# Kernel tuning notes

Measured on AMD Instinct MI355X. Metric: run time of the kernel, lower is better.

## Reference

```python
import jax, jax.numpy as jnp
import numpy as np

B, C_IN, C_OUT, A, H, W = 32, 256, 512, 256, 64, 64


def setup_inputs() -> dict:
    key = jax.random.key(0)
    ks = jax.random.split(key, 8)
    s = 0.02
    return {
        "x": jax.random.normal(ks[0], (B, C_IN, H, W), dtype=jnp.float32),
        "g": jax.random.normal(ks[1], (B, C_OUT), dtype=jnp.float32),
        "Wg": jax.random.normal(ks[2], (A, C_OUT), dtype=jnp.float32) * s,
        "bg": jnp.full((A,), 0.1, dtype=jnp.float32),
        "Wx": jax.random.normal(ks[3], (A, C_IN), dtype=jnp.float32) * s,
        "bx": jnp.full((A,), 0.1, dtype=jnp.float32),
        "Wf": jax.random.normal(ks[4], (1, A), dtype=jnp.float32) * s,
        "bf": jnp.full((1,), 0.1, dtype=jnp.float32),
    }


def reference(x, g, Wg, bg, Wx, bx, Wf, bf):
    b, c, h, w = x.shape
    gg = g @ Wg.T + bg                                  # [B, A]
    xf = x.reshape(b, c, h * w)                          # [B, C, HW]
    # Linear_x applied per spatial position (batched instead of python loop)
    nx = jnp.einsum('bcn,ac->bna', xf, Wx) + bx          # [B, HW, A]
    nx = jax.nn.relu(gg[:, None, :] + nx)                # [B, HW, A]
    att = jnp.einsum('bna,a->bn', nx, Wf[0]) + bf[0]     # [B, HW]
    # min-subtract, sum-divide normalization
    att = att - jnp.min(att, axis=1, keepdims=True)
    att = att / jnp.sum(att, axis=1, keepdims=True)
    out = jnp.einsum('bcn,bn->bc', xf, att)              # weighted pooling [B, C]
    return out, att.reshape(b, h, w)
```

## Files before the change

### kernel.cpp

```cpp
#include <hip/hip_runtime.h>
#include <stdint.h>

#define B_   32
#define CIN  256
#define COUT 512
#define A_   256
#define HW_  4096
#define NT   64

typedef short  short8  __attribute__((ext_vector_type(8)));
typedef float  float4_ __attribute__((ext_vector_type(4)));

__device__ __forceinline__ unsigned f2bf(float f) {
    unsigned u = __float_as_uint(f);
    u += 0x7FFFu + ((u >> 16) & 1u);
    return u >> 16;
}
__device__ __forceinline__ float bf2f(unsigned h) {
    return __uint_as_float(h << 16);
}

__global__ __launch_bounds__(256) void prep_kernel(
    const float* __restrict__ g, const float* __restrict__ Wg,
    const float* __restrict__ bg, const float* __restrict__ Wx,
    const float* __restrict__ bx,
    uint4* __restrict__ WxR, float* __restrict__ ggbx,
    float* __restrict__ P, float* __restrict__ T)
{
    int t = threadIdx.x;
    if (blockIdx.x >= 32) {
        int e = (blockIdx.x - 32) * 256 + t;
        int lane = e & 63, ai = (e >> 6) & 3, kk = (e >> 8) & 7, w = e >> 11;
        int a  = w * 64 + ai * 16 + (lane & 15);
        int kb = kk * 32 + (lane >> 4) * 8;
        const float4* s = (const float4*)(Wx + (size_t)a * 256 + kb);
        float4 u0 = s[0], u1 = s[1];
        uint4 pk;
        pk.x = f2bf(u0.x) | (f2bf(u0.y) << 16);
        pk.y = f2bf(u0.z) | (f2bf(u0.w) << 16);
        pk.z = f2bf(u1.x) | (f2bf(u1.y) << 16);
        pk.w = f2bf(u1.z) | (f2bf(u1.w) << 16);
        WxR[e] = pk;
        return;
    }
    int b = blockIdx.x;
    int i = b * 256 + t;
    P[i] = 0.f; T[i] = 0.f;

    __shared__ float gl[COUT];
    gl[t]       = g[b * COUT + t];
    gl[t + 256] = g[b * COUT + 256 + t];
    __syncthreads();

    float acc0 = bg[t] + bx[t], acc1 = 0.f;
    const float4* wr = (const float4*)(Wg + (size_t)t * COUT);
    #pragma unroll 8
    for (int co = 0; co < COUT / 4; co += 2) {
        float4 wv0 = wr[co],     gv0 = *(const float4*)&gl[co * 4];
        float4 wv1 = wr[co + 1], gv1 = *(const float4*)&gl[co * 4 + 4];
        acc0 += wv0.x * gv0.x + wv0.y * gv0.y + wv0.z * gv0.z + wv0.w * gv0.w;
        acc1 += wv1.x * gv1.x + wv1.y * gv1.y + wv1.z * gv1.z + wv1.w * gv1.w;
    }
    ggbx[b * 256 + t] = acc0 + acc1;
}

__global__ __launch_bounds__(256, 4) void attn_main(
    const float* __restrict__ x, const char* __restrict__ WxR,
    const float* __restrict__ ggbx, const float* __restrict__ Wf,
    const float* __restrict__ bfs,
    float* __restrict__ P, float* __restrict__ T, float* __restrict__ raw)
{
    __shared__ unsigned int xT[NT * 128];
    __shared__ float att_part[4][NT];
    __shared__ float raw_l[NT];

    int bid = blockIdx.x;
    int b = bid >> 6, nt = bid & 63;
    int t = threadIdx.x, w = t >> 6, lane = t & 63;
    int quad = lane >> 4, l15 = lane & 15;

    const float* xb = x + (size_t)b * CIN * HW_ + nt * NT;

    {
        int sub = lane >> 4;
        int n4  = (lane & 15) * 4;
        int cb0 = w * 64 + sub * 8;
        int cb1 = cb0 + 32;
        float4_ v[16];
        #pragma unroll
        for (int j = 0; j < 8; j++)
            v[j] = *(const float4_*)(xb + (size_t)(cb0 + j) * HW_ + n4);
        #pragma unroll
        for (int j = 0; j < 8; j++)
            v[8 + j] = *(const float4_*)(xb + (size_t)(cb1 + j) * HW_ + n4);

        #pragma unroll
        for (int gq = 0; gq < 2; gq++) {
            int q = (gq ? cb1 : cb0) >> 3;
            const float4_* vg = &v[gq * 8];
            #pragma unroll
            for (int r = 0; r < 4; r++) {
                uint4 pk;
                pk.x = f2bf(vg[0][r]) | (f2bf(vg[1][r]) << 16);
                pk.y = f2bf(vg[2][r]) | (f2bf(vg[3][r]) << 16);
                pk.z = f2bf(vg[4][r]) | (f2bf(vg[5][r]) << 16);
                pk.w = f2bf(vg[6][r]) | (f2bf(vg[7][r]) << 16);
                int n = n4 + r;
                *(uint4*)&xT[n * 128 + ((q ^ (n & 31)) << 2)] = pk;
            }
        }
    }

    float ga[4], wfv[4];
    #pragma unroll
    for (int ai = 0; ai < 4; ai++) {
        int a = w * 64 + ai * 16 + l15;
        ga[ai]  = ggbx[b * 256 + a];
        wfv[ai] = Wf[a];
    }
    __syncthreads();

    float4_ acc[4][4];
    #pragma unroll
    for (int mi = 0; mi < 4; mi++)
        #pragma unroll
        for (int ai = 0; ai < 4; ai++)
            acc[mi][ai] = (float4_){0.f, 0.f, 0.f, 0.f};

    const char* wsl = WxR + w * 32768 + lane * 16;
    short8 afA[4], bfA[4], afB[4], bfB[4];

    auto LD = [&](short8* af, short8* bf, int k0) {
        int qk = (k0 >> 3) + quad;
        #pragma unroll
        for (int mi = 0; mi < 4; mi++) {
            int n = mi * 16 + l15;
            af[mi] = *(const short8*)&xT[n * 128 + ((qk ^ (n & 31)) << 2)];
        }
        const char* wk = wsl + (k0 >> 5) * 4096;
        #pragma unroll
        for (int ai = 0; ai < 4; ai++)
            bf[ai] = *(const short8*)(wk + ai * 1024);
    };
    auto MM = [&](short8* af, short8* bf) {
        #pragma unroll
        for (int mi = 0; mi < 4; mi++)
            #pragma unroll
            for (int ai = 0; ai < 4; ai++)
                acc[mi][ai] = __builtin_amdgcn_mfma_f32_16x16x32_bf16(
                    af[mi], bf[ai], acc[mi][ai], 0, 0, 0);
    };

    LD(afA, bfA, 0);   LD(afB, bfB, 32);
    MM(afA, bfA);      LD(afA, bfA, 64);
    MM(afB, bfB);      LD(afB, bfB, 96);
    MM(afA, bfA);      LD(afA, bfA, 128);
    MM(afB, bfB);      LD(afB, bfB, 160);
    MM(afA, bfA);      LD(afA, bfA, 192);
    MM(afB, bfB);      LD(afB, bfB, 224);
    MM(afA, bfA);
    MM(afB, bfB);

    #pragma unroll
    for (int mi = 0; mi < 4; mi++) {
        float p[4] = {0.f, 0.f, 0.f, 0.f};
        #pragma unroll
        for (int ai = 0; ai < 4; ai++) {
            #pragma unroll
            for (int r = 0; r < 4; r++) {
                float vv = acc[mi][ai][r] + ga[ai];
                vv = fmaxf(vv, 0.f);
                p[r] = fmaf(vv, wfv[ai], p[r]);
            }
        }
        #pragma unroll
        for (int r = 0; r < 4; r++) {
            #pragma unroll
            for (int off = 1; off < 16; off <<= 1)
                p[r] += __shfl_xor(p[r], off, 16);
        }
        if (l15 == 0) {
            #pragma unroll
            for (int r = 0; r < 4; r++)
                att_part[w][mi * 16 + quad * 4 + r] = p[r];
        }
    }
    __syncthreads();

    if (t < NT) {
        float rv = att_part[0][t] + att_part[1][t] + att_part[2][t] + att_part[3][t] + bfs[0];
        raw[b * HW_ + nt * NT + t] = rv;
        raw_l[t] = rv;
    }
    __syncthreads();

    float pp[4] = {0.f, 0.f, 0.f, 0.f};
    float tt[4] = {0.f, 0.f, 0.f, 0.f};
    {
        int q    = (t & 63) >> 1;
        int half = (t & 1) * 8;
        int nb   = (t >> 6) * 16;
        #pragma unroll
        for (int i = 0; i < 16; i++) {
            int n = nb + i;
            uint2 u = *(const uint2*)((const char*)xT + n * 512 + ((q ^ (n & 31)) << 4) + half);
            float rv = raw_l[n];
            float x0 = bf2f(u.x & 0xFFFFu), x1 = bf2f(u.x >> 16);
            float x2 = bf2f(u.y & 0xFFFFu), x3 = bf2f(u.y >> 16);
            pp[0] = fmaf(x0, rv, pp[0]); tt[0] += x0;
            pp[1] = fmaf(x1, rv, pp[1]); tt[1] += x1;
            pp[2] = fmaf(x2, rv, pp[2]); tt[2] += x2;
            pp[3] = fmaf(x3, rv, pp[3]); tt[3] += x3;
        }
    }
    __syncthreads();
    {
        float* red = (float*)xT;
        float4_* pr = (float4_*)(red + w * 512);
        float4_* tr = (float4_*)(red + w * 512 + 256);
        pr[t & 63] = (float4_){pp[0], pp[1], pp[2], pp[3]};
        tr[t & 63] = (float4_){tt[0], tt[1], tt[2], tt[3]};
        __syncthreads();
        float Pc = red[t] + red[512 + t] + red[1024 + t] + red[1536 + t];
        float Tc = red[256 + t] + red[768 + t] + red[1280 + t] + red[1792 + t];
        atomicAdd(&P[b * 256 + t], Pc);
        atomicAdd(&T[b * 256 + t], Tc);
    }
}

__global__ __launch_bounds__(256) void finalize_kernel(
    const float* __restrict__ raw, const float* __restrict__ P,
    const float* __restrict__ T, float* __restrict__ out)
{
    int b = blockIdx.x, t = threadIdx.x;
    const float* r = raw + (size_t)b * HW_;
    float v[16];
    float mn = 3.4e38f, sm = 0.f;
    #pragma unroll
    for (int i = 0; i < 16; i++) {
        v[i] = r[t + 256 * i];
        mn = fminf(mn, v[i]);
        sm += v[i];
    }
    #pragma unroll
    for (int off = 1; off < 64; off <<= 1) {
        mn = fminf(mn, __shfl_xor(mn, off, 64));
        sm += __shfl_xor(sm, off, 64);
    }
    __shared__ float smn[4], ssm[4];
    int w = t >> 6;
    if ((t & 63) == 0) { smn[w] = mn; ssm[w] = sm; }
    __syncthreads();
    mn = fminf(fminf(smn[0], smn[1]), fminf(smn[2], smn[3]));
    sm = (ssm[0] + ssm[1]) + (ssm[2] + ssm[3]);
    float S = sm - 4096.f * mn;
    float inv = 1.f / S;

    float* att = out + B_ * CIN + (size_t)b * HW_;
    #pragma unroll
    for (int i = 0; i < 16; i++) att[t + 256 * i] = (v[i] - mn) * inv;

    int ic = b * 256 + t;
    out[ic] = (P[ic] - mn * T[ic]) * inv;
}

extern "C" void kernel_launch(void* const* d_in, const int* in_sizes, int n_in,
                              void* d_out, int out_size, void* d_ws, size_t ws_size,
                              hipStream_t stream)
{
    const float* x   = (const float*)d_in[0];
    const float* g   = (const float*)d_in[1];
    const float* Wg  = (const float*)d_in[2];
    const float* bg  = (const float*)d_in[3];
    const float* Wx  = (const float*)d_in[4];
    const float* bx  = (const float*)d_in[5];
    const float* Wf  = (const float*)d_in[6];
    const float* bf  = (const float*)d_in[7];
    float* out = (float*)d_out;

    char* wsb = (char*)d_ws;
    uint4* WxR  = (uint4*)wsb;
    float* ggbx = (float*)(wsb + 131072);
    float* P    = ggbx + 8192;
    float* T    = P + 8192;
    float* raw  = T + 8192;

    prep_kernel<<<64, 256, 0, stream>>>(g, Wg, bg, Wx, bx, WxR, ggbx, P, T);
    attn_main<<<2048, 256, 0, stream>>>(x, (const char*)WxR, ggbx, Wf, bf, P, T, raw);
    finalize_kernel<<<32, 256, 0, stream>>>(raw, P, T, out);
}
```

Measured before the change: 243.7 us.

## Make attention kernel persistent over 8 tiles with register-resident Wx and double-buffered x

Each block now handles 8 consecutive spatial tiles of 64 positions with 512 threads (8 waves) instead of one tile with 256 threads. Each wave keeps its slice of the bf16 Wx fragments in registers for the whole block rather than reloading them every tile. The next tile's x values are loaded into registers and written into a second LDS buffer while the current tile is processed, so global loads overlap compute. Per-block atomics to P and T also drop eightfold. In exchange the grid shrinks to 256 blocks, which lowers parallelism and occupancy on a large GPU, and register pressure rises.

```diff
diff --git a/kernel.cpp b/kernel.cpp
--- a/kernel.cpp
+++ b/kernel.cpp
@@ -7,6 +7,7 @@
 #define A_   256
 #define HW_  4096
 #define NT   64
+#define TILES 8
 
 typedef short  short8  __attribute__((ext_vector_type(8)));
 typedef float  float4_ __attribute__((ext_vector_type(4)));
@@ -64,146 +65,153 @@
     ggbx[b * 256 + t] = acc0 + acc1;
 }
 
-__global__ __launch_bounds__(256, 4) void attn_main(
+__global__ __launch_bounds__(512, 2) void attn_main(
     const float* __restrict__ x, const char* __restrict__ WxR,
     const float* __restrict__ ggbx, const float* __restrict__ Wf,
     const float* __restrict__ bfs,
     float* __restrict__ P, float* __restrict__ T, float* __restrict__ raw)
 {
-    __shared__ unsigned int xT[NT * 128];
-    __shared__ float att_part[4][NT];
+    __shared__ unsigned int xT[2][NT * 128];
+    __shared__ float att_part[8][NT];
     __shared__ float raw_l[NT];
 
     int bid = blockIdx.x;
-    int b = bid >> 6, nt = bid & 63;
+    int b = bid >> 3, tg = bid & 7;
     int t = threadIdx.x, w = t >> 6, lane = t & 63;
     int quad = lane >> 4, l15 = lane & 15;
 
-    const float* xb = x + (size_t)b * CIN * HW_ + nt * NT;
-
+    const float* xb = x + (size_t)b * CIN * HW_ + tg * (TILES * NT);
+
+    short8 bfp[16];
     {
-        int sub = lane >> 4;
-        int n4  = (lane & 15) * 4;
-        int cb0 = w * 64 + sub * 8;
-        int cb1 = cb0 + 32;
-        float4_ v[16];
-        #pragma unroll
-        for (int j = 0; j < 8; j++)
-            v[j] = *(const float4_*)(xb + (size_t)(cb0 + j) * HW_ + n4);
-        #pragma unroll
-        for (int j = 0; j < 8; j++)
-            v[8 + j] = *(const float4_*)(xb + (size_t)(cb1 + j) * HW_ + n4);
-
-        #pragma unroll
-        for (int gq = 0; gq < 2; gq++) {
-            int q = (gq ? cb1 : cb0) >> 3;
-            const float4_* vg = &v[gq * 8];
-            #pragma unroll
-            for (int r = 0; r < 4; r++) {
-                uint4 pk;
-                pk.x = f2bf(vg[0][r]) | (f2bf(vg[1][r]) << 16);
-                pk.y = f2bf(vg[2][r]) | (f2bf(vg[3][r]) << 16);
-                pk.z = f2bf(vg[4][r]) | (f2bf(vg[5][r]) << 16);
-                pk.w = f2bf(vg[6][r]) | (f2bf(vg[7][r]) << 16);
-                int n = n4 + r;
-                *(uint4*)&xT[n * 128 + ((q ^ (n & 31)) << 2)] = pk;
-            }
-        }
-    }
-
-    float ga[4], wfv[4];
-    #pragma unroll
-    for (int ai = 0; ai < 4; ai++) {
-        int a = w * 64 + ai * 16 + l15;
+        const char* wsl = WxR + (w >> 1) * 32768 + (w & 1) * 2048 + lane * 16;
+        #pragma unroll
+        for (int kk = 0; kk < 8; kk++) {
+            bfp[kk * 2]     = *(const short8*)(wsl + kk * 4096);
+            bfp[kk * 2 + 1] = *(const short8*)(wsl + kk * 4096 + 1024);
+        }
+    }
+
+    float ga[2], wfv[2];
+    #pragma unroll
+    for (int ai = 0; ai < 2; ai++) {
+        int a = w * 32 + ai * 16 + l15;
         ga[ai]  = ggbx[b * 256 + a];
         wfv[ai] = Wf[a];
     }
-    __syncthreads();
-
-    float4_ acc[4][4];
-    #pragma unroll
-    for (int mi = 0; mi < 4; mi++)
-        #pragma unroll
-        for (int ai = 0; ai < 4; ai++)
-            acc[mi][ai] = (float4_){0.f, 0.f, 0.f, 0.f};
-
-    const char* wsl = WxR + w * 32768 + lane * 16;
-    short8 afA[4], bfA[4], afB[4], bfB[4];
-
-    auto LD = [&](short8* af, short8* bf, int k0) {
-        int qk = (k0 >> 3) + quad;
-        #pragma unroll
-        for (int mi = 0; mi < 4; mi++) {
-            int n = mi * 16 + l15;
-            af[mi] = *(const short8*)&xT[n * 128 + ((qk ^ (n & 31)) << 2)];
-        }
-        const char* wk = wsl + (k0 >> 5) * 4096;
-        #pragma unroll
-        for (int ai = 0; ai < 4; ai++)
-            bf[ai] = *(const short8*)(wk + ai * 1024);
-    };
-    auto MM = [&](short8* af, short8* bf) {
-        #pragma unroll
-        for (int mi = 0; mi < 4; mi++)
-            #pragma unroll
-            for (int ai = 0; ai < 4; ai++)
-                acc[mi][ai] = __builtin_amdgcn_mfma_f32_16x16x32_bf16(
-                    af[mi], bf[ai], acc[mi][ai], 0, 0, 0);
-    };
-
-    LD(afA, bfA, 0);   LD(afB, bfB, 32);
-    MM(afA, bfA);      LD(afA, bfA, 64);
-    MM(afB, bfB);      LD(afB, bfB, 96);
-    MM(afA, bfA);      LD(afA, bfA, 128);
-    MM(afB, bfB);      LD(afB, bfB, 160);
-    MM(afA, bfA);      LD(afA, bfA, 192);
-    MM(afB, bfB);      LD(afB, bfB, 224);
-    MM(afA, bfA);
-    MM(afB, bfB);
-
-    #pragma unroll
-    for (int mi = 0; mi < 4; mi++) {
-        float p[4] = {0.f, 0.f, 0.f, 0.f};
-        #pragma unroll
-        for (int ai = 0; ai < 4; ai++) {
-            #pragma unroll
-            for (int r = 0; r < 4; r++) {
-                float vv = acc[mi][ai][r] + ga[ai];
-                vv = fmaxf(vv, 0.f);
-                p[r] = fmaf(vv, wfv[ai], p[r]);
-            }
-        }
-        #pragma unroll
-        for (int r = 0; r < 4; r++) {
-            #pragma unroll
-            for (int off = 1; off < 16; off <<= 1)
-                p[r] += __shfl_xor(p[r], off, 16);
-        }
-        if (l15 == 0) {
-            #pragma unroll
-            for (int r = 0; r < 4; r++)
-                att_part[w][mi * 16 + quad * 4 + r] = p[r];
-        }
-    }
-    __syncthreads();
-
-    if (t < NT) {
-        float rv = att_part[0][t] + att_part[1][t] + att_part[2][t] + att_part[3][t] + bfs[0];
-        raw[b * HW_ + nt * NT + t] = rv;
-        raw_l[t] = rv;
-    }
-    __syncthreads();
+
+    int n4 = l15 * 4;
+    int cb = w * 32 + quad * 8;
+    int qc = cb >> 3;
+    const float* xrow = xb + (size_t)cb * HW_ + n4;
+
+    float4_ v[8];
+    #pragma unroll
+    for (int j = 0; j < 8; j++)
+        v[j] = *(const float4_*)(xrow + (size_t)j * HW_);
+    #pragma unroll
+    for (int r = 0; r < 4; r++) {
+        uint4 pk;
+        pk.x = f2bf(v[0][r]) | (f2bf(v[1][r]) << 16);
+        pk.y = f2bf(v[2][r]) | (f2bf(v[3][r]) << 16);
+        pk.z = f2bf(v[4][r]) | (f2bf(v[5][r]) << 16);
+        pk.w = f2bf(v[6][r]) | (f2bf(v[7][r]) << 16);
+        int n = n4 + r;
+        *(uint4*)&xT[0][n * 128 + ((qc ^ (n & 31)) << 2)] = pk;
+    }
 
     float pp[4] = {0.f, 0.f, 0.f, 0.f};
     float tt[4] = {0.f, 0.f, 0.f, 0.f};
-    {
-        int q    = (t & 63) >> 1;
-        int half = (t & 1) * 8;
-        int nb   = (t >> 6) * 16;
-        #pragma unroll
-        for (int i = 0; i < 16; i++) {
-            int n = nb + i;
-            uint2 u = *(const uint2*)((const char*)xT + n * 512 + ((q ^ (n & 31)) << 4) + half);
+    int qpt   = (t & 63) >> 1;
+    int half  = (t & 1) * 8;
+    int nbase = w * 8;
+
+    __syncthreads();
+
+    #pragma unroll
+    for (int it = 0; it < TILES; it++) {
+        const unsigned int* xl = xT[it & 1];
+
+        if (it < TILES - 1) {
+            const float* xn = xrow + (it + 1) * NT;
+            #pragma unroll
+            for (int j = 0; j < 8; j++)
+                v[j] = *(const float4_*)(xn + (size_t)j * HW_);
+        }
+
+        float4_ acc[4][2];
+        #pragma unroll
+        for (int mi = 0; mi < 4; mi++) {
+            acc[mi][0] = (float4_){0.f, 0.f, 0.f, 0.f};
+            acc[mi][1] = (float4_){0.f, 0.f, 0.f, 0.f};
+        }
+        short8 afA[4], afB[4];
+        auto LDA = [&](short8* af, int k0) {
+            int qk = (k0 >> 3) + quad;
+            #pragma unroll
+            for (int mi = 0; mi < 4; mi++) {
+                int n = mi * 16 + l15;
+                af[mi] = *(const short8*)&xl[n * 128 + ((qk ^ (n & 31)) << 2)];
+            }
+        };
+        auto MM = [&](short8* af, int ks) {
+            #pragma unroll
+            for (int mi = 0; mi < 4; mi++) {
+                acc[mi][0] = __builtin_amdgcn_mfma_f32_16x16x32_bf16(
+                    af[mi], bfp[ks * 2],     acc[mi][0], 0, 0, 0);
+                acc[mi][1] = __builtin_amdgcn_mfma_f32_16x16x32_bf16(
+                    af[mi], bfp[ks * 2 + 1], acc[mi][1], 0, 0, 0);
+            }
+        };
+
+        LDA(afA, 0);   LDA(afB, 32);
+        MM(afA, 0);    LDA(afA, 64);
+        MM(afB, 1);    LDA(afB, 96);
+        MM(afA, 2);    LDA(afA, 128);
+        MM(afB, 3);    LDA(afB, 160);
+        MM(afA, 4);    LDA(afA, 192);
+        MM(afB, 5);    LDA(afB, 224);
+        MM(afA, 6);
+        MM(afB, 7);
+
+        #pragma unroll
+        for (int mi = 0; mi < 4; mi++) {
+            float p[4] = {0.f, 0.f, 0.f, 0.f};
+            #pragma unroll
+            for (int ai = 0; ai < 2; ai++) {
+                #pragma unroll
+                for (int r = 0; r < 4; r++) {
+                    float vv = fmaxf(acc[mi][ai][r] + ga[ai], 0.f);
+                    p[r] = fmaf(vv, wfv[ai], p[r]);
+                }
+            }
+            #pragma unroll
+            for (int r = 0; r < 4; r++) {
+                #pragma unroll
+                for (int off = 1; off < 16; off <<= 1)
+                    p[r] += __shfl_xor(p[r], off, 16);
+            }
+            if (l15 == 0) {
+                #pragma unroll
+                for (int r = 0; r < 4; r++)
+                    att_part[w][mi * 16 + quad * 4 + r] = p[r];
+            }
+        }
+        __syncthreads();
+
+        if (t < NT) {
+            float rv = att_part[0][t] + att_part[1][t] + att_part[2][t] + att_part[3][t]
+                     + att_part[4][t] + att_part[5][t] + att_part[6][t] + att_part[7][t]
+                     + bfs[0];
+            raw[b * HW_ + (tg * TILES + it) * NT + t] = rv;
+            raw_l[t] = rv;
+        }
+        __syncthreads();
+
+        #pragma unroll
+        for (int i = 0; i < 8; i++) {
+            int n = nbase + i;
+            uint2 u = *(const uint2*)((const char*)xl + n * 512 + ((qpt ^ (n & 31)) << 4) + half);
             float rv = raw_l[n];
             float x0 = bf2f(u.x & 0xFFFFu), x1 = bf2f(u.x >> 16);
             float x2 = bf2f(u.y & 0xFFFFu), x3 = bf2f(u.y >> 16);
@@ -212,19 +220,35 @@
             pp[2] = fmaf(x2, rv, pp[2]); tt[2] += x2;
             pp[3] = fmaf(x3, rv, pp[3]); tt[3] += x3;
         }
-    }
-    __syncthreads();
+
+        if (it < TILES - 1) {
+            #pragma unroll
+            for (int r = 0; r < 4; r++) {
+                uint4 pk;
+                pk.x = f2bf(v[0][r]) | (f2bf(v[1][r]) << 16);
+                pk.y = f2bf(v[2][r]) | (f2bf(v[3][r]) << 16);
+                pk.z = f2bf(v[4][r]) | (f2bf(v[5][r]) << 16);
+                pk.w = f2bf(v[6][r]) | (f2bf(v[7][r]) << 16);
+                int n = n4 + r;
+                *(uint4*)&xT[(it + 1) & 1][n * 128 + ((qc ^ (n & 31)) << 2)] = pk;
+            }
+        }
+        __syncthreads();
+    }
+
     {
         float* red = (float*)xT;
         float4_* pr = (float4_*)(red + w * 512);
         float4_* tr = (float4_*)(red + w * 512 + 256);
-        pr[t & 63] = (float4_){pp[0], pp[1], pp[2], pp[3]};
-        tr[t & 63] = (float4_){tt[0], tt[1], tt[2], tt[3]};
+        pr[lane] = (float4_){pp[0], pp[1], pp[2], pp[3]};
+        tr[lane] = (float4_){tt[0], tt[1], tt[2], tt[3]};
         __syncthreads();
-        float Pc = red[t] + red[512 + t] + red[1024 + t] + red[1536 + t];
-        float Tc = red[256 + t] + red[768 + t] + red[1280 + t] + red[1792 + t];
-        atomicAdd(&P[b * 256 + t], Pc);
-        atomicAdd(&T[b * 256 + t], Tc);
+        int sel = t >> 8, cc = t & 255;
+        float s = 0.f;
+        #pragma unroll
+        for (int g = 0; g < 8; g++)
+            s += red[g * 512 + sel * 256 + cc];
+        atomicAdd((sel ? T : P) + b * 256 + cc, s);
     }
 }
 
@@ -286,6 +310,6 @@
     float* raw  = T + 8192;
 
     prep_kernel<<<64, 256, 0, stream>>>(g, Wg, bg, Wx, bx, WxR, ggbx, P, T);
-    attn_main<<<2048, 256, 0, stream>>>(x, (const char*)WxR, ggbx, Wf, bf, P, T, raw);
+    attn_main<<<256, 512, 0, stream>>>(x, (const char*)WxR, ggbx, Wf, bf, P, T, raw);
     finalize_kernel<<<32, 256, 0, stream>>>(raw, P, T, out);
 }
```

Result: slower. 253.2 us (+3.9%).
